# Optimization experiments

Hardware: AMD Instinct MI355X
Metric: run time of the kernel (lower is better)

Reference implementation:

```python
import jax, jax.numpy as jnp
import numpy as np

REF_POSE = np.array([[213.33335876464844, 124.50563049316406], [190.504638671875, 115.11840057373047], [169.9791717529297, 101.77180480957031], [146.72341918945312, 96.25749206542969], [128.86770629882812, 87.2344970703125], [150.34292602539062, 101.61070251464844], [119.29926300048828, 98.73982238769531], [100.03463745117188, 99.74459838867188], [82.62400817871094, 101.2509536743164], [148.91049194335938, 112.71517181396484], [114.37303161621094, 113.20121002197266], [91.90096282958984, 116.49812316894531], [74.75020599365234, 119.37875366210938], [149.59658813476562, 124.09295654296875], [119.72419738769531, 126.36898040771484], [99.59107208251953, 129.40196228027344], [82.82524108886719, 131.584228515625], [154.55911254882812, 135.07681274414062], [133.8833770751953, 140.85983276367188], [120.45906066894531, 145.40306091308594], [106.21541595458984, 150.072265625]], dtype=np.float32)

SCALES = (0.25, 0.5, 1.0)
ORIENTATIONS = (0, 90, 180, 270)
INPUT_SIZE = (256, 256)          # (H, W)
ANCHOR_STRIDE = (1, 1)           # (y_stride, x_stride)
POS_TH = 0.5
KPT_SIGMA = 0.05                 # per-keypoint OKS falloff


def _generate_anchor_poses():
    # scale + rotate ref pose about its centroid -> [A, 21, 2]
    c = REF_POSE.mean(axis=0, keepdims=True)
    out = []
    for s in SCALES:
        for o in ORIENTATIONS:
            th = np.deg2rad(o)
            R = np.array([[np.cos(th), -np.sin(th)], [np.sin(th), np.cos(th)]], dtype=np.float32)
            out.append(c + s * (REF_POSE - c) @ R.T)
    return np.stack(out).astype(np.float32)


def _all_anchors(feat_h, feat_w):
    base = _generate_anchor_poses()                      # [A,21,2]
    w_ratio = INPUT_SIZE[1] / feat_w
    h_ratio = INPUT_SIZE[0] / feat_h
    sx = np.arange(0, feat_w, ANCHOR_STRIDE[1]) * w_ratio
    sy = np.arange(0, feat_h, ANCHOR_STRIDE[0]) * h_ratio
    gx, gy = np.meshgrid(sx, sy)
    shifts = np.stack([gx.ravel(), gy.ravel()], axis=1).astype(np.float32)  # [K,2]
    all_a = base[None, :, :, :] + shifts[:, None, None, :]                  # [K,A,21,2]
    return jnp.asarray(all_a.reshape(-1, 21, 2))                            # [K*A,21,2]


def _pose_oks(anchors, gt):
    # anchors [N,21,2], gt [B,2,21,3] -> OKS sim [B,N,2]
    d2 = jnp.sum((anchors[None, :, None, :, :] - gt[:, None, :, :, :2]) ** 2, axis=-1)  # [B,N,2,21]
    vis = (gt[..., 2] > 0).astype(anchors.dtype)[:, None, :, :]                          # [B,1,2,21]
    xy = gt[..., :2]
    area = jnp.prod(xy.max(axis=2) - xy.min(axis=2), axis=-1)                            # [B,2]
    s2 = jnp.maximum(area, 1.0)[:, None, :, None]                                        # [B,1,2,1]
    k2 = (2.0 * KPT_SIGMA) ** 2
    oks = jnp.exp(-d2 / (2.0 * s2 * k2))
    return jnp.sum(oks * vis, axis=-1) / jnp.maximum(jnp.sum(vis, axis=-1), 1.0)          # [B,N,2]


def setup_inputs() -> dict:
    key = jax.random.key(0)
    k1, k2 = jax.random.split(key)
    B = 16
    xy = jax.random.uniform(k1, (B, 42, 2), dtype=jnp.float32) * 216.0 + 20.0
    vis = jnp.ones((B, 42, 1), dtype=jnp.float32)
    pose_gt = jnp.concatenate([xy, vis], axis=-1)          # [B,42,3]
    hand_type = jnp.ones((B, 2), dtype=jnp.int32)          # both hands present
    return {"pose_gt": pose_gt, "hand_type": hand_type, "feat_h": 64, "feat_w": 64}


def reference(pose_gt, hand_type, feat_h, feat_w):
    all_anchors = _all_anchors(feat_h, feat_w)             # [N,21,2], N=K*A
    inside = jnp.sum((all_anchors[..., 0] >= 0) & (all_anchors[..., 1] >= 0)
                     & (all_anchors[..., 0] < INPUT_SIZE[0])
                     & (all_anchors[..., 1] < INPUT_SIZE[1]), axis=1) == 21  # [N]

    B = pose_gt.shape[0]
    gt = pose_gt.reshape(B, 2, 21, 3)                      # hand 0 = right, hand 1 = left
    sim = _pose_oks(all_anchors, gt)                       # [B,N,2]
    am = jnp.argmax(sim, axis=-1)                          # [B,N]
    mx = jnp.max(sim, axis=-1)                             # [B,N]

    right = (am == 0) & (mx > POS_TH) & (hand_type[:, 0:1] == 1) & inside[None, :]
    left = (am == 1) & (mx > POS_TH) & (hand_type[:, 1:2] == 1) & inside[None, :]
    neg = (~right) & (~left) & inside[None, :]

    # labels channel layout matches source: [:,:,0]=left, [:,:,1]=negative, [:,:,2]=right
    labels = jnp.stack([left, neg, right], axis=-1).astype(pose_gt.dtype)   # [B,N,3]
    labels = jnp.where(inside[None, :, None], labels, jnp.asarray(-1.0, pose_gt.dtype))

    pose_targets = (jnp.where(right[..., None, None], gt[:, 0][:, None], 0.0)
                    + jnp.where(left[..., None, None], gt[:, 1][:, None], 0.0))  # [B,N,21,3]

    offsets = pose_targets[..., :2] - all_anchors[None, :, :, :]             # [B,N,21,2]
    offsets = jnp.where(inside[None, :, None, None], offsets, 0.0)
    return all_anchors, inside, labels, offsets
```

## Files before the change

kernel.cpp:

```cpp
#include <hip/hip_runtime.h>
#include <math.h>

#define NA 49152
#define NB 16
#define ABLOCKS 192
#define EPS 1e-3f

__device__ __forceinline__ void st4(float* p, float a, float b, float c, float d) {
  *reinterpret_cast<float4*>(p) = make_float4(a, b, c, d);
}

__constant__ float RP[21][2] = {
  {213.33335876464844f, 124.50563049316406f},
  {190.504638671875f,   115.11840057373047f},
  {169.9791717529297f,  101.77180480957031f},
  {146.72341918945312f, 96.25749206542969f},
  {128.86770629882812f, 87.2344970703125f},
  {150.34292602539062f, 101.61070251464844f},
  {119.29926300048828f, 98.73982238769531f},
  {100.03463745117188f, 99.74459838867188f},
  {82.62400817871094f,  101.2509536743164f},
  {148.91049194335938f, 112.71517181396484f},
  {114.37303161621094f, 113.20121002197266f},
  {91.90096282958984f,  116.49812316894531f},
  {74.75020599365234f,  119.37875366210938f},
  {149.59658813476562f, 124.09295654296875f},
  {119.72419738769531f, 126.36898040771484f},
  {99.59107208251953f,  129.40196228027344f},
  {82.82524108886719f,  131.584228515625f},
  {154.55911254882812f, 135.07681274414062f},
  {133.8833770751953f,  140.85983276367188f},
  {120.45906066894531f, 145.40306091308594f},
  {106.21541595458984f, 150.072265625f}
};

__device__ __forceinline__ void ref_center(float& cx, float& cy) {
  #pragma clang fp contract(off)
  float rx[8], ry[8];
  #pragma unroll
  for (int j = 0; j < 8; ++j) {
    rx[j] = RP[j][0] + RP[j + 8][0];
    ry[j] = RP[j][1] + RP[j + 8][1];
  }
  float sx = ((rx[0] + rx[1]) + (rx[2] + rx[3])) + ((rx[4] + rx[5]) + (rx[6] + rx[7]));
  float sy = ((ry[0] + ry[1]) + (ry[2] + ry[3])) + ((ry[4] + ry[5]) + (ry[6] + ry[7]));
  #pragma unroll
  for (int j = 16; j < 21; ++j) { sx += RP[j][0]; sy += RP[j][1]; }
  cx = sx / 21.0f;
  cy = sy / 21.0f;
}

__device__ __forceinline__ float2 base_pt(int p, int j, float cx, float cy) {
  #pragma clang fp contract(off)
  const int si = p >> 2, oi = p & 3;
  const float s = (si == 0) ? 0.25f : (si == 1 ? 0.5f : 1.0f);
  const float dx = s * (RP[j][0] - cx);
  const float dy = s * (RP[j][1] - cy);
  const float rx = (oi == 0) ? dx : (oi == 1 ? -dy : (oi == 2 ? -dx : dy));
  const float ry = (oi == 0) ? dy : (oi == 1 ? dx : (oi == 2 ? -dy : -dx));
  return make_float2(cx + rx, cy + ry);
}

__global__ __launch_bounds__(256, 5) void k_all(const float* __restrict__ gt,
                                                const int* __restrict__ ht,
                                                float* __restrict__ oa,
                                                float* __restrict__ oins,
                                                float* __restrict__ ol,
                                                float* __restrict__ oo) {
  __shared__ float2 sb2[252];
  __shared__ float4 sg4[21];
  __shared__ float2 sv2[21];
  __shared__ float sden[2], srden[2], snv[2];
  __shared__ int sht[2];
  __shared__ float4 sanc[256];

  const int tid = threadIdx.x;
  const int b = blockIdx.x / ABLOCKS;
  const int ab = blockIdx.x % ABLOCKS;
  const int a0 = ab * 256;

  if (tid < 252) {
    float cx, cy; ref_center(cx, cy);
    sb2[tid] = base_pt(tid / 21, tid % 21, cx, cy);
  }
  if (tid < 21) {
    const float* g0 = gt + b * 126 + tid * 3;
    const float* g1 = g0 + 63;
    sg4[tid] = make_float4(g0[0], g0[1], g1[0], g1[1]);
    sv2[tid] = make_float2((g0[2] > 0.0f) ? 1.0f : 0.0f,
                           (g1[2] > 0.0f) ? 1.0f : 0.0f);
  }
  if (tid == 252 || tid == 253) {
    const int h = tid - 252;
    const float* g = gt + b * 126 + h * 63;
    float mnx = g[0], mxx = g[0], mny = g[1], mxy = g[1];
    float nv = (g[2] > 0.0f) ? 1.0f : 0.0f;
    for (int j = 1; j < 21; ++j) {
      float x = g[j * 3], y = g[j * 3 + 1];
      mnx = fminf(mnx, x); mxx = fmaxf(mxx, x);
      mny = fminf(mny, y); mxy = fmaxf(mxy, y);
      nv += (g[j * 3 + 2] > 0.0f) ? 1.0f : 0.0f;
    }
    const float area = (mxx - mnx) * (mxy - mny);
    const float s2 = fmaxf(area, 1.0f);
    const float den = (2.0f * s2) * 0.01f;
    sden[h] = den;
    srden[h] = -1.0f / den;
    snv[h] = fmaxf(nv, 1.0f);
  }
  if (tid == 254 || tid == 255) sht[tid - 254] = ht[b * 2 + (tid - 254)];
  __syncthreads();

  const int a = a0 + tid;
  const int p = a % 12;
  const int kc = a / 12;
  const float shx = 4.0f * (float)(kc & 63);
  const float shy = 4.0f * (float)(kc >> 6);
  const int pb = p * 21;

  const float rd0 = srden[0], rd1 = srden[1];
  bool inside = true;
  float s0f = 0.0f, s1f = 0.0f;
  #pragma unroll
  for (int j = 0; j < 21; ++j) {
    #pragma clang fp contract(off)
    const float2 bpv = sb2[pb + j];
    const float anx = bpv.x + shx;
    const float any = bpv.y + shy;
    inside = inside && (anx >= 0.0f) && (any >= 0.0f) &&
                       (anx < 256.0f) && (any < 256.0f);
    const float4 g = sg4[j];
    const float2 v = sv2[j];
    const float dx0 = anx - g.x, dy0 = any - g.y;
    const float dx1 = anx - g.z, dy1 = any - g.w;
    s0f += __expf((dx0 * dx0 + dy0 * dy0) * rd0) * v.x;
    s1f += __expf((dx1 * dx1 + dy1 * dy1) * rd1) * v.y;
  }
  float sim0 = s0f / snv[0];
  float sim1 = s1f / snv[1];
  const float mxf = fmaxf(sim0, sim1);
  const bool need_exact = (fabsf(mxf - 0.5f) < EPS) ||
                          ((mxf > 0.5f - EPS) && (fabsf(sim0 - sim1) < EPS));

  if (__builtin_expect(need_exact, 0)) {
    #pragma clang fp contract(off)
    float q0[8], q1[8];
    #pragma unroll
    for (int j = 0; j < 16; ++j) {
      const float2 bpv = sb2[pb + j];
      const float ax = bpv.x + shx, ay = bpv.y + shy;
      const float4 g = sg4[j];
      const float2 v = sv2[j];
      float dx0 = ax - g.x, dy0 = ay - g.y;
      float d20 = dx0 * dx0 + dy0 * dy0;
      float t0 = (float)::exp((double)(-d20 / sden[0])) * v.x;
      float dx1 = ax - g.z, dy1 = ay - g.w;
      float d21 = dx1 * dx1 + dy1 * dy1;
      float t1 = (float)::exp((double)(-d21 / sden[1])) * v.y;
      if (j < 8) { q0[j] = t0; q1[j] = t1; }
      else       { q0[j - 8] += t0; q1[j - 8] += t1; }
    }
    float s0 = ((q0[0] + q0[1]) + (q0[2] + q0[3])) + ((q0[4] + q0[5]) + (q0[6] + q0[7]));
    float s1 = ((q1[0] + q1[1]) + (q1[2] + q1[3])) + ((q1[4] + q1[5]) + (q1[6] + q1[7]));
    #pragma unroll
    for (int j = 16; j < 21; ++j) {
      const float2 bpv = sb2[pb + j];
      const float ax = bpv.x + shx, ay = bpv.y + shy;
      const float4 g = sg4[j];
      const float2 v = sv2[j];
      float dx0 = ax - g.x, dy0 = ay - g.y;
      float d20 = dx0 * dx0 + dy0 * dy0;
      s0 += (float)::exp((double)(-d20 / sden[0])) * v.x;
      float dx1 = ax - g.z, dy1 = ay - g.w;
      float d21 = dx1 * dx1 + dy1 * dy1;
      s1 += (float)::exp((double)(-d21 / sden[1])) * v.y;
    }
    sim0 = s0 / snv[0];
    sim1 = s1 / snv[1];
  }

  const int am = (sim1 > sim0) ? 1 : 0;
  const float mx = fmaxf(sim0, sim1);
  const bool pos = mx > 0.5f;
  const bool right = (am == 0) && pos && (sht[0] == 1) && inside;
  const bool left  = (am == 1) && pos && (sht[1] == 1) && inside;

  int c;
  if (!inside)      c = -1;
  else if (right)   c = 1;
  else if (left)    c = 2;
  else              c = 0;
  sanc[tid] = make_float4(shx, shy, (float)pb, (float)c);
  __syncthreads();

  if (tid < 192) {
    float* lb = ol + ((size_t)b * NA + a0) * 3;
    float r[4];
    #pragma unroll
    for (int k = 0; k < 4; ++k) {
      const int q = tid * 4 + k;
      const int al = q / 3;
      const int rr = q - al * 3;
      const int cc = (int)sanc[al].w;
      float v;
      if (cc < 0)       v = -1.0f;
      else if (rr == 0) v = (cc == 2) ? 1.0f : 0.0f;
      else if (rr == 1) v = (cc == 0) ? 1.0f : 0.0f;
      else              v = (cc == 1) ? 1.0f : 0.0f;
      r[k] = v;
    }
    st4(lb + tid * 4, r[0], r[1], r[2], r[3]);
  }

  {
    float* ob = oo + ((size_t)b * NA + a0) * 42;
    int al = (2 * tid) / 21;
    int jj = 2 * tid - al * 21;
    #pragma unroll
    for (int i = 0; i < 11; ++i) {
      #pragma clang fp contract(off)
      if (i == 10 && tid >= 128) break;
      const int idx = i * 256 + tid;
      const bool w1 = (jj + 1) >= 21;
      const int al1 = al + (w1 ? 1 : 0);
      const int j1 = w1 ? 0 : (jj + 1);
      float r[4];
      {
        const float4 sa = sanc[al];
        const int cc = (int)sa.w;
        const float2 bpv = sb2[(int)sa.z + jj];
        const float anx = bpv.x + sa.x, any = bpv.y + sa.y;
        const float4 g = sg4[jj];
        const bool has = (cc == 1) || (cc == 2);
        float tx = (cc == 2) ? g.z : g.x;
        float ty = (cc == 2) ? g.w : g.y;
        tx = has ? tx : 0.0f; ty = has ? ty : 0.0f;
        r[0] = (cc >= 0) ? (tx - anx) : 0.0f;
        r[1] = (cc >= 0) ? (ty - any) : 0.0f;
      }
      {
        const float4 sa = sanc[al1];
        const int cc = (int)sa.w;
        const float2 bpv = sb2[(int)sa.z + j1];
        const float anx = bpv.x + sa.x, any = bpv.y + sa.y;
        const float4 g = sg4[j1];
        const bool has = (cc == 1) || (cc == 2);
        float tx = (cc == 2) ? g.z : g.x;
        float ty = (cc == 2) ? g.w : g.y;
        tx = has ? tx : 0.0f; ty = has ? ty : 0.0f;
        r[2] = (cc >= 0) ? (tx - anx) : 0.0f;
        r[3] = (cc >= 0) ? (ty - any) : 0.0f;
      }
      st4(ob + idx * 4, r[0], r[1], r[2], r[3]);
      jj += 8; al += 24;
      if (jj >= 21) { jj -= 21; ++al; }
    }
  }

  if (tid < 168) {
    float* ap = oa + (size_t)a0 * 42;
    const int idx = b * 168 + tid;
    const int e0 = idx * 2;
    const int al = e0 / 21;
    const int jj = e0 - al * 21;
    const bool w1 = (jj + 1) >= 21;
    const int al1 = al + (w1 ? 1 : 0);
    const int j1 = w1 ? 0 : (jj + 1);
    const float4 sa = sanc[al];
    const float2 bpv = sb2[(int)sa.z + jj];
    const float4 sb = sanc[al1];
    const float2 bq = sb2[(int)sb.z + j1];
    st4(ap + idx * 4, bpv.x + sa.x, bpv.y + sa.y,
                      bq.x + sb.x,  bq.y + sb.y);
  }
  if (tid < 4) {
    const int t = b * 4 + tid;
    st4(oins + a0 + t * 4,
        (sanc[t * 4].w     >= 0.0f) ? 1.0f : 0.0f,
        (sanc[t * 4 + 1].w >= 0.0f) ? 1.0f : 0.0f,
        (sanc[t * 4 + 2].w >= 0.0f) ? 1.0f : 0.0f,
        (sanc[t * 4 + 3].w >= 0.0f) ? 1.0f : 0.0f);
  }
}

extern "C" void kernel_launch(void* const* d_in, const int* in_sizes, int n_in,
                              void* d_out, int out_size, void* d_ws, size_t ws_size,
                              hipStream_t stream) {
  (void)in_sizes; (void)n_in; (void)d_ws; (void)ws_size; (void)out_size;
  const float* gt = (const float*)d_in[0];
  const int* ht = (const int*)d_in[1];
  float* out = (float*)d_out;
  float* out_anchors = out;
  float* out_inside  = out + (size_t)NA * 42;
  float* out_labels  = out + (size_t)NA * 43;
  float* out_offsets = out_labels + (size_t)NB * NA * 3;

  hipLaunchKernelGGL(k_all, dim3(NB * ABLOCKS), dim3(256), 0, stream,
                     gt, ht, out_anchors, out_inside, out_labels, out_offsets);
}
```

Baseline: 159.9 us.

## Process 3072-anchor chunks per 1024-thread block to amortize per-block setup

Each block now handles 3072 anchors with 1024 threads, and each thread computes three anchors. The grid shrinks from 3072 blocks to 256. The goal is to amortize the per-block shared-memory setup (base poses, GT staging, per-hand statistics) across more anchors. In exchange, the grid now holds exactly one block per CU on a 256-CU part, and the large blocks lose the latency hiding that many small blocks gave, which could hurt the store-bound output phase.

```diff
diff --git a/kernel.cpp b/kernel.cpp
--- a/kernel.cpp
+++ b/kernel.cpp
@@ -3,7 +3,7 @@
 
 #define NA 49152
 #define NB 16
-#define ABLOCKS 192
+#define CHUNK 3072
 #define EPS 1e-3f
 
 __device__ __forceinline__ void st4(float* p, float a, float b, float c, float d) {
@@ -61,23 +61,23 @@
   return make_float2(cx + rx, cy + ry);
 }
 
-__global__ __launch_bounds__(256, 5) void k_all(const float* __restrict__ gt,
-                                                const int* __restrict__ ht,
-                                                float* __restrict__ oa,
-                                                float* __restrict__ oins,
-                                                float* __restrict__ ol,
-                                                float* __restrict__ oo) {
+__global__ __launch_bounds__(1024, 4) void k_all(const float* __restrict__ gt,
+                                                 const int* __restrict__ ht,
+                                                 float* __restrict__ oa,
+                                                 float* __restrict__ oins,
+                                                 float* __restrict__ ol,
+                                                 float* __restrict__ oo) {
   __shared__ float2 sb2[252];
   __shared__ float4 sg4[21];
   __shared__ float2 sv2[21];
   __shared__ float sden[2], srden[2], snv[2];
   __shared__ int sht[2];
-  __shared__ float4 sanc[256];
+  __shared__ float4 sanc[CHUNK];
 
   const int tid = threadIdx.x;
-  const int b = blockIdx.x / ABLOCKS;
-  const int ab = blockIdx.x % ABLOCKS;
-  const int a0 = ab * 256;
+  const int b = blockIdx.x >> 4;
+  const int c = blockIdx.x & 15;
+  const int A0 = c * CHUNK;
 
   if (tid < 252) {
     float cx, cy; ref_center(cx, cy);
@@ -111,116 +111,124 @@
   if (tid == 254 || tid == 255) sht[tid - 254] = ht[b * 2 + (tid - 254)];
   __syncthreads();
 
-  const int a = a0 + tid;
-  const int p = a % 12;
-  const int kc = a / 12;
-  const float shx = 4.0f * (float)(kc & 63);
-  const float shy = 4.0f * (float)(kc >> 6);
-  const int pb = p * 21;
-
   const float rd0 = srden[0], rd1 = srden[1];
-  bool inside = true;
-  float s0f = 0.0f, s1f = 0.0f;
   #pragma unroll
-  for (int j = 0; j < 21; ++j) {
-    #pragma clang fp contract(off)
-    const float2 bpv = sb2[pb + j];
-    const float anx = bpv.x + shx;
-    const float any = bpv.y + shy;
-    inside = inside && (anx >= 0.0f) && (any >= 0.0f) &&
-                       (anx < 256.0f) && (any < 256.0f);
-    const float4 g = sg4[j];
-    const float2 v = sv2[j];
-    const float dx0 = anx - g.x, dy0 = any - g.y;
-    const float dx1 = anx - g.z, dy1 = any - g.w;
-    s0f += __expf((dx0 * dx0 + dy0 * dy0) * rd0) * v.x;
-    s1f += __expf((dx1 * dx1 + dy1 * dy1) * rd1) * v.y;
-  }
-  float sim0 = s0f / snv[0];
-  float sim1 = s1f / snv[1];
-  const float mxf = fmaxf(sim0, sim1);
-  const bool need_exact = (fabsf(mxf - 0.5f) < EPS) ||
-                          ((mxf > 0.5f - EPS) && (fabsf(sim0 - sim1) < EPS));
-
-  if (__builtin_expect(need_exact, 0)) {
-    #pragma clang fp contract(off)
-    float q0[8], q1[8];
+  for (int k = 0; k < 3; ++k) {
+    const int aloc = k * 1024 + tid;
+    const int a = A0 + aloc;
+    const int p = a % 12;
+    const int kc = a / 12;
+    const float shx = 4.0f * (float)(kc & 63);
+    const float shy = 4.0f * (float)(kc >> 6);
+    const int pb = p * 21;
+
+    bool inside = true;
+    float s0f = 0.0f, s1f = 0.0f;
     #pragma unroll
-    for (int j = 0; j < 16; ++j) {
+    for (int j = 0; j < 21; ++j) {
+      #pragma clang fp contract(off)
       const float2 bpv = sb2[pb + j];
-      const float ax = bpv.x + shx, ay = bpv.y + shy;
+      const float anx = bpv.x + shx;
+      const float any = bpv.y + shy;
+      inside = inside && (anx >= 0.0f) && (any >= 0.0f) &&
+                         (anx < 256.0f) && (any < 256.0f);
       const float4 g = sg4[j];
       const float2 v = sv2[j];
-      float dx0 = ax - g.x, dy0 = ay - g.y;
-      float d20 = dx0 * dx0 + dy0 * dy0;
-      float t0 = (float)::exp((double)(-d20 / sden[0])) * v.x;
-      float dx1 = ax - g.z, dy1 = ay - g.w;
-      float d21 = dx1 * dx1 + dy1 * dy1;
-      float t1 = (float)::exp((double)(-d21 / sden[1])) * v.y;
-      if (j < 8) { q0[j] = t0; q1[j] = t1; }
-      else       { q0[j - 8] += t0; q1[j - 8] += t1; }
-    }
-    float s0 = ((q0[0] + q0[1]) + (q0[2] + q0[3])) + ((q0[4] + q0[5]) + (q0[6] + q0[7]));
-    float s1 = ((q1[0] + q1[1]) + (q1[2] + q1[3])) + ((q1[4] + q1[5]) + (q1[6] + q1[7]));
+      const float dx0 = anx - g.x, dy0 = any - g.y;
+      const float dx1 = anx - g.z, dy1 = any - g.w;
+      s0f += __expf((dx0 * dx0 + dy0 * dy0) * rd0) * v.x;
+      s1f += __expf((dx1 * dx1 + dy1 * dy1) * rd1) * v.y;
+    }
+    float sim0 = s0f / snv[0];
+    float sim1 = s1f / snv[1];
+    const float mxf = fmaxf(sim0, sim1);
+    const bool need_exact = (fabsf(mxf - 0.5f) < EPS) ||
+                            ((mxf > 0.5f - EPS) && (fabsf(sim0 - sim1) < EPS));
+
+    if (__builtin_expect(need_exact, 0)) {
+      #pragma clang fp contract(off)
+      float q0[8], q1[8];
+      #pragma unroll
+      for (int j = 0; j < 16; ++j) {
+        const float2 bpv = sb2[pb + j];
+        const float ax = bpv.x + shx, ay = bpv.y + shy;
+        const float4 g = sg4[j];
+        const float2 v = sv2[j];
+        float dx0 = ax - g.x, dy0 = ay - g.y;
+        float d20 = dx0 * dx0 + dy0 * dy0;
+        float t0 = (float)::exp((double)(-d20 / sden[0])) * v.x;
+        float dx1 = ax - g.z, dy1 = ay - g.w;
+        float d21 = dx1 * dx1 + dy1 * dy1;
+        float t1 = (float)::exp((double)(-d21 / sden[1])) * v.y;
+        if (j < 8) { q0[j] = t0; q1[j] = t1; }
+        else       { q0[j - 8] += t0; q1[j - 8] += t1; }
+      }
+      float s0 = ((q0[0] + q0[1]) + (q0[2] + q0[3])) + ((q0[4] + q0[5]) + (q0[6] + q0[7]));
+      float s1 = ((q1[0] + q1[1]) + (q1[2] + q1[3])) + ((q1[4] + q1[5]) + (q1[6] + q1[7]));
+      #pragma unroll
+      for (int j = 16; j < 21; ++j) {
+        const float2 bpv = sb2[pb + j];
+        const float ax = bpv.x + shx, ay = bpv.y + shy;
+        const float4 g = sg4[j];
+        const float2 v = sv2[j];
+        float dx0 = ax - g.x, dy0 = ay - g.y;
+        float d20 = dx0 * dx0 + dy0 * dy0;
+        s0 += (float)::exp((double)(-d20 / sden[0])) * v.x;
+        float dx1 = ax - g.z, dy1 = ay - g.w;
+        float d21 = dx1 * dx1 + dy1 * dy1;
+        s1 += (float)::exp((double)(-d21 / sden[1])) * v.y;
+      }
+      sim0 = s0 / snv[0];
+      sim1 = s1 / snv[1];
+    }
+
+    const int am = (sim1 > sim0) ? 1 : 0;
+    const float mx = fmaxf(sim0, sim1);
+    const bool pos = mx > 0.5f;
+    const bool right = (am == 0) && pos && (sht[0] == 1) && inside;
+    const bool left  = (am == 1) && pos && (sht[1] == 1) && inside;
+
+    int cdec;
+    if (!inside)      cdec = -1;
+    else if (right)   cdec = 1;
+    else if (left)    cdec = 2;
+    else              cdec = 0;
+    sanc[aloc] = make_float4(shx, shy, (float)pb, (float)cdec);
+  }
+  __syncthreads();
+
+  {
+    float* lb = ol + ((size_t)b * NA + A0) * 3;
     #pragma unroll
-    for (int j = 16; j < 21; ++j) {
-      const float2 bpv = sb2[pb + j];
-      const float ax = bpv.x + shx, ay = bpv.y + shy;
-      const float4 g = sg4[j];
-      const float2 v = sv2[j];
-      float dx0 = ax - g.x, dy0 = ay - g.y;
-      float d20 = dx0 * dx0 + dy0 * dy0;
-      s0 += (float)::exp((double)(-d20 / sden[0])) * v.x;
-      float dx1 = ax - g.z, dy1 = ay - g.w;
-      float d21 = dx1 * dx1 + dy1 * dy1;
-      s1 += (float)::exp((double)(-d21 / sden[1])) * v.y;
-    }
-    sim0 = s0 / snv[0];
-    sim1 = s1 / snv[1];
-  }
-
-  const int am = (sim1 > sim0) ? 1 : 0;
-  const float mx = fmaxf(sim0, sim1);
-  const bool pos = mx > 0.5f;
-  const bool right = (am == 0) && pos && (sht[0] == 1) && inside;
-  const bool left  = (am == 1) && pos && (sht[1] == 1) && inside;
-
-  int c;
-  if (!inside)      c = -1;
-  else if (right)   c = 1;
-  else if (left)    c = 2;
-  else              c = 0;
-  sanc[tid] = make_float4(shx, shy, (float)pb, (float)c);
-  __syncthreads();
-
-  if (tid < 192) {
-    float* lb = ol + ((size_t)b * NA + a0) * 3;
-    float r[4];
+    for (int i = 0; i < 3; ++i) {
+      if (i == 2 && tid >= 256) break;
+      const int idx = i * 1024 + tid;
+      float r[4];
+      #pragma unroll
+      for (int kk = 0; kk < 4; ++kk) {
+        const int q = idx * 4 + kk;
+        const int al = q / 3;
+        const int rr = q - al * 3;
+        const int cc = (int)sanc[al].w;
+        float v;
+        if (cc < 0)       v = -1.0f;
+        else if (rr == 0) v = (cc == 2) ? 1.0f : 0.0f;
+        else if (rr == 1) v = (cc == 0) ? 1.0f : 0.0f;
+        else              v = (cc == 1) ? 1.0f : 0.0f;
+        r[kk] = v;
+      }
+      st4(lb + idx * 4, r[0], r[1], r[2], r[3]);
+    }
+  }
+
+  {
+    float* ob = oo + ((size_t)b * NA + A0) * 42;
+    int al = (2 * tid) / 21;
+    int jj = (2 * tid) - al * 21;
     #pragma unroll
-    for (int k = 0; k < 4; ++k) {
-      const int q = tid * 4 + k;
-      const int al = q / 3;
-      const int rr = q - al * 3;
-      const int cc = (int)sanc[al].w;
-      float v;
-      if (cc < 0)       v = -1.0f;
-      else if (rr == 0) v = (cc == 2) ? 1.0f : 0.0f;
-      else if (rr == 1) v = (cc == 0) ? 1.0f : 0.0f;
-      else              v = (cc == 1) ? 1.0f : 0.0f;
-      r[k] = v;
-    }
-    st4(lb + tid * 4, r[0], r[1], r[2], r[3]);
-  }
-
-  {
-    float* ob = oo + ((size_t)b * NA + a0) * 42;
-    int al = (2 * tid) / 21;
-    int jj = 2 * tid - al * 21;
-    #pragma unroll
-    for (int i = 0; i < 11; ++i) {
-      #pragma clang fp contract(off)
-      if (i == 10 && tid >= 128) break;
-      const int idx = i * 256 + tid;
+    for (int i = 0; i < 32; ++i) {
+      if (i == 31 && tid >= 512) break;
+      const int idx = i * 1024 + tid;
       const bool w1 = (jj + 1) >= 21;
       const int al1 = al + (w1 ? 1 : 0);
       const int j1 = w1 ? 0 : (jj + 1);
@@ -252,30 +260,34 @@
         r[3] = (cc >= 0) ? (ty - any) : 0.0f;
       }
       st4(ob + idx * 4, r[0], r[1], r[2], r[3]);
-      jj += 8; al += 24;
+      jj += 11; al += 97;
       if (jj >= 21) { jj -= 21; ++al; }
     }
   }
 
-  if (tid < 168) {
-    float* ap = oa + (size_t)a0 * 42;
-    const int idx = b * 168 + tid;
-    const int e0 = idx * 2;
-    const int al = e0 / 21;
-    const int jj = e0 - al * 21;
-    const bool w1 = (jj + 1) >= 21;
-    const int al1 = al + (w1 ? 1 : 0);
-    const int j1 = w1 ? 0 : (jj + 1);
-    const float4 sa = sanc[al];
-    const float2 bpv = sb2[(int)sa.z + jj];
-    const float4 sb = sanc[al1];
-    const float2 bq = sb2[(int)sb.z + j1];
-    st4(ap + idx * 4, bpv.x + sa.x, bpv.y + sa.y,
-                      bq.x + sb.x,  bq.y + sb.y);
-  }
-  if (tid < 4) {
-    const int t = b * 4 + tid;
-    st4(oins + a0 + t * 4,
+  {
+    float* ap = oa + (size_t)A0 * 42;
+    #pragma unroll
+    for (int i = 0; i < 2; ++i) {
+      if (i == 1 && tid >= 992) break;
+      const int idx = b * 2016 + i * 1024 + tid;
+      const int e0 = idx * 2;
+      const int al = e0 / 21;
+      const int jj = e0 - al * 21;
+      const bool w1 = (jj + 1) >= 21;
+      const int al1 = al + (w1 ? 1 : 0);
+      const int j1 = w1 ? 0 : (jj + 1);
+      const float4 sa = sanc[al];
+      const float2 bpv = sb2[(int)sa.z + jj];
+      const float4 sb = sanc[al1];
+      const float2 bq = sb2[(int)sb.z + j1];
+      st4(ap + idx * 4, bpv.x + sa.x, bpv.y + sa.y,
+                        bq.x + sb.x,  bq.y + sb.y);
+    }
+  }
+  if (tid < 48) {
+    const int t = b * 48 + tid;
+    st4(oins + A0 + t * 4,
         (sanc[t * 4].w     >= 0.0f) ? 1.0f : 0.0f,
         (sanc[t * 4 + 1].w >= 0.0f) ? 1.0f : 0.0f,
         (sanc[t * 4 + 2].w >= 0.0f) ? 1.0f : 0.0f,
@@ -295,6 +307,6 @@
   float* out_labels  = out + (size_t)NA * 43;
   float* out_offsets = out_labels + (size_t)NB * NA * 3;
 
-  hipLaunchKernelGGL(k_all, dim3(NB * ABLOCKS), dim3(256), 0, stream,
+  hipLaunchKernelGGL(k_all, dim3(NB * 16), dim3(1024), 0, stream,
                      gt, ht, out_anchors, out_inside, out_labels, out_offsets);
 }
```

Result: slower. 171.0 us (+7.0%).

## Split fused kernel into decision pass and grid-stride output streaming pass

Applied to the files above, without the earlier changes.

The single kernel is split in two. The first computes the per-anchor similarity decisions and writes the labels plus a byte code per (batch, anchor) to workspace. The second, a persistent grid-stride kernel, streams the large offsets, anchors and inside outputs using recomputed anchor coordinates and those codes. The aim is to decouple the compute-heavy OKS phase from the store-bound phase so writes run at full bandwidth, at the cost of a second launch and a small extra round trip through global memory for the codes.

```diff
diff --git a/kernel.cpp b/kernel.cpp
--- a/kernel.cpp
+++ b/kernel.cpp
@@ -5,6 +5,10 @@
 #define NB 16
 #define ABLOCKS 192
 #define EPS 1e-3f
+#define OF4B 516096
+#define OF4  8257536
+#define AF4  516096
+#define IF4  12288
 
 __device__ __forceinline__ void st4(float* p, float a, float b, float c, float d) {
   *reinterpret_cast<float4*>(p) = make_float4(a, b, c, d);
@@ -61,18 +65,16 @@
   return make_float2(cx + rx, cy + ry);
 }
 
-__global__ __launch_bounds__(256, 5) void k_all(const float* __restrict__ gt,
-                                                const int* __restrict__ ht,
-                                                float* __restrict__ oa,
-                                                float* __restrict__ oins,
-                                                float* __restrict__ ol,
-                                                float* __restrict__ oo) {
+__global__ __launch_bounds__(256, 5) void k_decide(const float* __restrict__ gt,
+                                                   const int* __restrict__ ht,
+                                                   float* __restrict__ ol,
+                                                   char* __restrict__ codes) {
   __shared__ float2 sb2[252];
   __shared__ float4 sg4[21];
   __shared__ float2 sv2[21];
   __shared__ float sden[2], srden[2], snv[2];
   __shared__ int sht[2];
-  __shared__ float4 sanc[256];
+  __shared__ int scc[256];
 
   const int tid = threadIdx.x;
   const int b = blockIdx.x / ABLOCKS;
@@ -190,7 +192,8 @@
   else if (right)   c = 1;
   else if (left)    c = 2;
   else              c = 0;
-  sanc[tid] = make_float4(shx, shy, (float)pb, (float)c);
+  scc[tid] = c;
+  codes[b * NA + a] = (char)c;
   __syncthreads();
 
   if (tid < 192) {
@@ -201,7 +204,7 @@
       const int q = tid * 4 + k;
       const int al = q / 3;
       const int rr = q - al * 3;
-      const int cc = (int)sanc[al].w;
+      const int cc = scc[al];
       float v;
       if (cc < 0)       v = -1.0f;
       else if (rr == 0) v = (cc == 2) ? 1.0f : 0.0f;
@@ -211,82 +214,95 @@
     }
     st4(lb + tid * 4, r[0], r[1], r[2], r[3]);
   }
-
-  {
-    float* ob = oo + ((size_t)b * NA + a0) * 42;
-    int al = (2 * tid) / 21;
-    int jj = 2 * tid - al * 21;
-    #pragma unroll
-    for (int i = 0; i < 11; ++i) {
-      #pragma clang fp contract(off)
-      if (i == 10 && tid >= 128) break;
-      const int idx = i * 256 + tid;
-      const bool w1 = (jj + 1) >= 21;
-      const int al1 = al + (w1 ? 1 : 0);
-      const int j1 = w1 ? 0 : (jj + 1);
-      float r[4];
-      {
-        const float4 sa = sanc[al];
-        const int cc = (int)sa.w;
-        const float2 bpv = sb2[(int)sa.z + jj];
-        const float anx = bpv.x + sa.x, any = bpv.y + sa.y;
-        const float4 g = sg4[jj];
-        const bool has = (cc == 1) || (cc == 2);
-        float tx = (cc == 2) ? g.z : g.x;
-        float ty = (cc == 2) ? g.w : g.y;
-        tx = has ? tx : 0.0f; ty = has ? ty : 0.0f;
-        r[0] = (cc >= 0) ? (tx - anx) : 0.0f;
-        r[1] = (cc >= 0) ? (ty - any) : 0.0f;
-      }
-      {
-        const float4 sa = sanc[al1];
-        const int cc = (int)sa.w;
-        const float2 bpv = sb2[(int)sa.z + j1];
-        const float anx = bpv.x + sa.x, any = bpv.y + sa.y;
-        const float4 g = sg4[j1];
-        const bool has = (cc == 1) || (cc == 2);
-        float tx = (cc == 2) ? g.z : g.x;
-        float ty = (cc == 2) ? g.w : g.y;
-        tx = has ? tx : 0.0f; ty = has ? ty : 0.0f;
-        r[2] = (cc >= 0) ? (tx - anx) : 0.0f;
-        r[3] = (cc >= 0) ? (ty - any) : 0.0f;
-      }
-      st4(ob + idx * 4, r[0], r[1], r[2], r[3]);
-      jj += 8; al += 24;
-      if (jj >= 21) { jj -= 21; ++al; }
-    }
-  }
-
-  if (tid < 168) {
-    float* ap = oa + (size_t)a0 * 42;
-    const int idx = b * 168 + tid;
-    const int e0 = idx * 2;
-    const int al = e0 / 21;
-    const int jj = e0 - al * 21;
-    const bool w1 = (jj + 1) >= 21;
-    const int al1 = al + (w1 ? 1 : 0);
-    const int j1 = w1 ? 0 : (jj + 1);
-    const float4 sa = sanc[al];
-    const float2 bpv = sb2[(int)sa.z + jj];
-    const float4 sb = sanc[al1];
-    const float2 bq = sb2[(int)sb.z + j1];
-    st4(ap + idx * 4, bpv.x + sa.x, bpv.y + sa.y,
-                      bq.x + sb.x,  bq.y + sb.y);
-  }
-  if (tid < 4) {
-    const int t = b * 4 + tid;
-    st4(oins + a0 + t * 4,
-        (sanc[t * 4].w     >= 0.0f) ? 1.0f : 0.0f,
-        (sanc[t * 4 + 1].w >= 0.0f) ? 1.0f : 0.0f,
-        (sanc[t * 4 + 2].w >= 0.0f) ? 1.0f : 0.0f,
-        (sanc[t * 4 + 3].w >= 0.0f) ? 1.0f : 0.0f);
+}
+
+__device__ __forceinline__ float2 off_elem(int e, const char* __restrict__ codes,
+                                           int cb, const float2* sb2,
+                                           const float4* sg) {
+  #pragma clang fp contract(off)
+  const int al = e / 21;
+  const int j  = e - al * 21;
+  const int kc = al / 12;
+  const int p  = al - kc * 12;
+  const float shx = 4.0f * (float)(kc & 63);
+  const float shy = 4.0f * (float)(kc >> 6);
+  const float2 bpv = sb2[p * 21 + j];
+  const float anx = bpv.x + shx, any = bpv.y + shy;
+  const int cc = (int)codes[cb + al];
+  const float4 g = sg[j];
+  const bool has = (cc == 1) || (cc == 2);
+  float tx = (cc == 2) ? g.z : g.x;
+  float ty = (cc == 2) ? g.w : g.y;
+  tx = has ? tx : 0.0f; ty = has ? ty : 0.0f;
+  return make_float2((cc >= 0) ? (tx - anx) : 0.0f,
+                     (cc >= 0) ? (ty - any) : 0.0f);
+}
+
+__device__ __forceinline__ float2 anc_elem(int e, const float2* sb2) {
+  const int al = e / 21;
+  const int j  = e - al * 21;
+  const int kc = al / 12;
+  const int p  = al - kc * 12;
+  const float shx = 4.0f * (float)(kc & 63);
+  const float shy = 4.0f * (float)(kc >> 6);
+  const float2 bpv = sb2[p * 21 + j];
+  return make_float2(bpv.x + shx, bpv.y + shy);
+}
+
+__global__ __launch_bounds__(256, 6) void k_stream(const float* __restrict__ gt,
+                                                   const char* __restrict__ codes,
+                                                   float* __restrict__ oa,
+                                                   float* __restrict__ oins,
+                                                   float* __restrict__ oo) {
+  __shared__ float2 sb2[252];
+  __shared__ float4 sgall[NB * 21];
+
+  const int tid = threadIdx.x;
+  if (tid < 252) {
+    float cx, cy; ref_center(cx, cy);
+    sb2[tid] = base_pt(tid / 21, tid % 21, cx, cy);
+  }
+  for (int t = tid; t < NB * 21; t += 256) {
+    const int bb = t / 21, j = t - bb * 21;
+    const float* g0 = gt + bb * 126 + j * 3;
+    const float* g1 = g0 + 63;
+    sgall[t] = make_float4(g0[0], g0[1], g1[0], g1[1]);
+  }
+  __syncthreads();
+
+  const int G = gridDim.x * 256;
+  const int g0i = blockIdx.x * 256 + tid;
+
+  for (int q = g0i; q < OF4; q += G) {
+    const int b = q / OF4B;
+    const int r = q - b * OF4B;
+    const int e0 = 2 * r;
+    const float2 r0 = off_elem(e0,     codes, b * NA, sb2, sgall + b * 21);
+    const float2 r1 = off_elem(e0 + 1, codes, b * NA, sb2, sgall + b * 21);
+    st4(oo + (size_t)q * 4, r0.x, r0.y, r1.x, r1.y);
+  }
+
+  for (int q = g0i; q < AF4; q += G) {
+    const int e0 = 2 * q;
+    const float2 r0 = anc_elem(e0, sb2);
+    const float2 r1 = anc_elem(e0 + 1, sb2);
+    st4(oa + (size_t)q * 4, r0.x, r0.y, r1.x, r1.y);
+  }
+
+  for (int q = g0i; q < IF4; q += G) {
+    const char4 c4 = *reinterpret_cast<const char4*>(codes + q * 4);
+    st4(oins + (size_t)q * 4,
+        (c4.x >= 0) ? 1.0f : 0.0f,
+        (c4.y >= 0) ? 1.0f : 0.0f,
+        (c4.z >= 0) ? 1.0f : 0.0f,
+        (c4.w >= 0) ? 1.0f : 0.0f);
   }
 }
 
 extern "C" void kernel_launch(void* const* d_in, const int* in_sizes, int n_in,
                               void* d_out, int out_size, void* d_ws, size_t ws_size,
                               hipStream_t stream) {
-  (void)in_sizes; (void)n_in; (void)d_ws; (void)ws_size; (void)out_size;
+  (void)in_sizes; (void)n_in; (void)ws_size; (void)out_size;
   const float* gt = (const float*)d_in[0];
   const int* ht = (const int*)d_in[1];
   float* out = (float*)d_out;
@@ -294,7 +310,10 @@
   float* out_inside  = out + (size_t)NA * 42;
   float* out_labels  = out + (size_t)NA * 43;
   float* out_offsets = out_labels + (size_t)NB * NA * 3;
-
-  hipLaunchKernelGGL(k_all, dim3(NB * ABLOCKS), dim3(256), 0, stream,
-                     gt, ht, out_anchors, out_inside, out_labels, out_offsets);
-}
+  char* codes = (char*)d_ws;
+
+  hipLaunchKernelGGL(k_decide, dim3(NB * ABLOCKS), dim3(256), 0, stream,
+                     gt, ht, out_labels, codes);
+  hipLaunchKernelGGL(k_stream, dim3(2048), dim3(256), 0, stream,
+                     gt, codes, out_anchors, out_inside, out_offsets);
+}
```

Measured after the change: 171.0 us. +7.0%, slower.
